# Optimization experiments

Measured on AMD Instinct MI355X. Metric: run time of the kernel, lower is better.

Reference implementation:

```python
import jax, jax.numpy as jnp
import numpy as np

N, S, C, K, V = 8, 2048, 4, 512, 64


def setup_inputs() -> dict:
    key = jax.random.key(0)
    kx, ke = jax.random.split(key)
    x = jax.random.normal(kx, (N, S, C, V), dtype=jnp.float32)
    # nn.Parameter(torch.rand(...)) -> uniform [0,1)
    embedding = jax.random.uniform(ke, (C, K, V), dtype=jnp.float32)
    return {"x": x, "embedding": embedding}


def reference(x, embedding):
    n, s, c, v = x.shape
    xf = x.reshape(n * s, c, v)  # (NS, C, V)
    x2 = jnp.sum(xf * xf, axis=-1, keepdims=True)           # (NS, C, 1)
    e2 = jnp.sum(embedding * embedding, axis=-1)            # (C, K)
    xe = jnp.einsum('ncv,ckv->nck', xf, embedding)          # (NS, C, K)
    d2 = x2 - 2.0 * xe + e2[None]                           # (NS, C, K)
    index = jnp.argmin(d2, axis=2)                          # (NS, C)
    # gather: output[n, c] = embedding[c, index[n, c]]
    output = embedding[jnp.arange(c)[None, :], index]       # (NS, C, V)
    output = output.reshape(x.shape)
    out0 = jax.lax.stop_gradient(output - x) + x            # straight-through
    d1 = jax.lax.stop_gradient(x) - output
    out1 = jnp.sum(d1 * d1, axis=3)                         # (N, S, C)
    d2_ = x - jax.lax.stop_gradient(output)
    out2 = jnp.sum(d2_ * d2_, axis=3)                       # (N, S, C)
    return (out0, out1, out2)
```

## Files before the change

kernel.cpp:

```cpp
#include <hip/hip_runtime.h>

#define NROW 16384
#define CCH  4
#define KCB  512
#define VDIM 64

typedef __attribute__((ext_vector_type(8))) short  short8;
typedef __attribute__((ext_vector_type(4))) float  floatx4;

__device__ inline unsigned short bf16h(float v, float* rem) {
    unsigned u = __float_as_uint(v);
    unsigned r = u + 0x7FFFu + ((u >> 16) & 1u);
    unsigned short h = (unsigned short)(r >> 16);
    *rem = v - __uint_as_float((unsigned)h << 16);
    return h;
}
__device__ inline unsigned short bf16r(float v) {
    unsigned u = __float_as_uint(v);
    return (unsigned short)((u + 0x7FFFu + ((u >> 16) & 1u)) >> 16);
}

__global__ __launch_bounds__(512, 4)
void vq_fused(const float* __restrict__ x, const float* __restrict__ emb,
              float* __restrict__ out) {
    extern __shared__ unsigned short smem[];
    unsigned short* eh = smem;
    float* e2s = (float*)(smem + 32768);

    const int tid  = threadIdx.x;
    const int lane = tid & 63;
    const int m    = lane & 15;
    const int quad = lane >> 4;
    const int wave = tid >> 6;
    const int c    = blockIdx.y;
    const int rbase = blockIdx.x * 128 + wave * 16;

    const float* embc = emb + (size_t)c * (KCB * VDIM);

    {
        const int cb = wave * 64;
        const int koct = m >> 1, half = m & 1;
#pragma unroll
        for (int j = 0; j < 16; ++j) {
            const int g = cb * 16 + j * 64 + lane;
            const float4 t = ((const float4*)embc)[g];
            const int code = cb + j * 4 + quad;
            ushort4 h4;
            h4.x = bf16r(t.x); h4.y = bf16r(t.y);
            h4.z = bf16r(t.z); h4.w = bf16r(t.w);
            const int off = (koct * 512 + (code ^ koct)) * 8 + half * 4;
            *(ushort4*)&eh[off] = h4;
            float s = 0.f;
            s = fmaf(t.x, t.x, s); s = fmaf(t.y, t.y, s);
            s = fmaf(t.z, t.z, s); s = fmaf(t.w, t.w, s);
            s += __shfl_xor(s, 1, 64);
            s += __shfl_xor(s, 2, 64);
            s += __shfl_xor(s, 4, 64);
            s += __shfl_xor(s, 8, 64);
            if (m == 0) e2s[code] = s;
        }
    }

    short8 ah[2], al[2];
    {
        const int row = rbase + m;
        const float4* xr = (const float4*)(x + ((size_t)row * CCH + c) * VDIM);
#pragma unroll
        for (int h = 0; h < 2; ++h) {
            const float4 f0 = xr[h * 8 + quad * 2];
            const float4 f1 = xr[h * 8 + quad * 2 + 1];
            const float fv[8] = {f0.x, f0.y, f0.z, f0.w, f1.x, f1.y, f1.z, f1.w};
            short8 hh, ll;
#pragma unroll
            for (int j = 0; j < 8; ++j) {
                float r, d;
                hh[j] = (short)bf16h(fv[j], &r);
                ll[j] = (short)bf16h(r, &d);
            }
            ah[h] = hh; al[h] = ll;
        }
    }

    __syncthreads();

    float bd[4]; int bkk[4];
#pragma unroll
    for (int j = 0; j < 4; ++j) { bd[j] = 3.4e38f; bkk[j] = 0; }

    const int mq0 = m ^ quad;
    const int mq1 = m ^ (quad + 4);

#pragma unroll 4
    for (int t = 0; t < KCB / 16; ++t) {
        const int code = t * 16 + m;
        const short8 bh0 = *(const short8*)&eh[( quad      * 512 + t * 16 + mq0) * 8];
        const short8 bh1 = *(const short8*)&eh[((quad + 4) * 512 + t * 16 + mq1) * 8];
        const float e2v = e2s[code];

        floatx4 acc0 = {0.f,0.f,0.f,0.f}, acc1 = {0.f,0.f,0.f,0.f};
        acc0 = __builtin_amdgcn_mfma_f32_16x16x32_bf16(ah[0], bh0, acc0, 0, 0, 0);
        acc1 = __builtin_amdgcn_mfma_f32_16x16x32_bf16(al[0], bh0, acc1, 0, 0, 0);
        acc0 = __builtin_amdgcn_mfma_f32_16x16x32_bf16(ah[1], bh1, acc0, 0, 0, 0);
        acc1 = __builtin_amdgcn_mfma_f32_16x16x32_bf16(al[1], bh1, acc1, 0, 0, 0);

#pragma unroll
        for (int j = 0; j < 4; ++j) {
            const float d0 = fmaf(-2.0f, acc0[j] + acc1[j], e2v);
            if (d0 < bd[j]) { bd[j] = d0; bkk[j] = code; }
        }
    }

#pragma unroll
    for (int j = 0; j < 4; ++j) {
        float d = bd[j]; int k = bkk[j];
#pragma unroll
        for (int mask = 1; mask < 16; mask <<= 1) {
            const float od = __shfl_xor(d, mask, 64);
            const int   ok = __shfl_xor(k, mask, 64);
            if (od < d || (od == d && ok < k)) { d = od; k = ok; }
        }
        bd[j] = d; bkk[j] = k;
    }

    const size_t base1 = (size_t)NROW * CCH * VDIM;
    const size_t base2 = base1 + (size_t)NROW * CCH;
#pragma unroll
    for (int j = 0; j < 4; ++j) {
        const int row  = rbase + quad * 4 + j;
        const int code = bkk[j];
        const float4 t4 = ((const float4*)(x + ((size_t)row * CCH + c) * VDIM))[m];
        const float4 e4 = ((const float4*)(embc + (size_t)code * VDIM))[m];
        float4 w;
        w.x = (e4.x - t4.x) + t4.x;
        w.y = (e4.y - t4.y) + t4.y;
        w.z = (e4.z - t4.z) + t4.z;
        w.w = (e4.w - t4.w) + t4.w;
        ((float4*)(out + ((size_t)row * CCH + c) * VDIM))[m] = w;
        float s = 0.f, dx;
        dx = t4.x - e4.x; s = fmaf(dx, dx, s);
        dx = t4.y - e4.y; s = fmaf(dx, dx, s);
        dx = t4.z - e4.z; s = fmaf(dx, dx, s);
        dx = t4.w - e4.w; s = fmaf(dx, dx, s);
        s += __shfl_xor(s, 1, 64);
        s += __shfl_xor(s, 2, 64);
        s += __shfl_xor(s, 4, 64);
        s += __shfl_xor(s, 8, 64);
        if (m == 0) {
            const size_t idx = (size_t)row * CCH + c;
            out[base1 + idx] = s;
            out[base2 + idx] = s;
        }
    }
}

extern "C" void kernel_launch(void* const* d_in, const int* in_sizes, int n_in,
                              void* d_out, int out_size, void* d_ws, size_t ws_size,
                              hipStream_t stream) {
    const float* x   = (const float*)d_in[0];
    const float* emb = (const float*)d_in[1];
    float* out = (float*)d_out;
    const size_t lds_bytes = 65536u + 2048u;
    vq_fused<<<dim3(NROW / 128, CCH), dim3(512), lds_bytes, stream>>>(x, emb, out);
}
```

Before: 85.33 us.

## Split codebook search across two wave groups per row tile and merge via LDS

Each block now handles 64 rows instead of 128, and its eight waves form two groups that each scan half of the codebook (256 codes) for the same 16-row tiles. The two partial argmin results go through shared memory, and the first group merges them and writes the outputs. This halves the serial codebook loop per wave and doubles the grid. The cost is that every block still converts and stages the full codebook into LDS, so that staging work is done twice as often overall, plus an extra barrier. The x row fragments are also loaded twice.

```diff
diff --git a/kernel.cpp b/kernel.cpp
--- a/kernel.cpp
+++ b/kernel.cpp
@@ -23,17 +23,21 @@
 __global__ __launch_bounds__(512, 4)
 void vq_fused(const float* __restrict__ x, const float* __restrict__ emb,
               float* __restrict__ out) {
-    extern __shared__ unsigned short smem[];
-    unsigned short* eh = smem;
-    float* e2s = (float*)(smem + 32768);
+    extern __shared__ char smem[];
+    unsigned short* eh  = (unsigned short*)smem;
+    float*          e2s = (float*)(smem + 65536);
+    float*          sdm = (float*)(smem + 67584);
+    int*            skm = (int*)  (smem + 68096);
 
     const int tid  = threadIdx.x;
     const int lane = tid & 63;
     const int m    = lane & 15;
     const int quad = lane >> 4;
     const int wave = tid >> 6;
+    const int z    = wave >> 2;
+    const int wb   = wave & 3;
     const int c    = blockIdx.y;
-    const int rbase = blockIdx.x * 128 + wave * 16;
+    const int rbase = blockIdx.x * 64 + wb * 16;
 
     const float* embc = emb + (size_t)c * (KCB * VDIM);
 
@@ -87,14 +91,15 @@
 #pragma unroll
     for (int j = 0; j < 4; ++j) { bd[j] = 3.4e38f; bkk[j] = 0; }
 
-    const int mq0 = m ^ quad;
-    const int mq1 = m ^ (quad + 4);
+    const int mq0 = m ^ quad, mq1 = m ^ (quad + 4);
+    const int kbase = z * 256;
 
 #pragma unroll 4
-    for (int t = 0; t < KCB / 16; ++t) {
-        const int code = t * 16 + m;
-        const short8 bh0 = *(const short8*)&eh[( quad      * 512 + t * 16 + mq0) * 8];
-        const short8 bh1 = *(const short8*)&eh[((quad + 4) * 512 + t * 16 + mq1) * 8];
+    for (int t = 0; t < 16; ++t) {
+        const int kb = kbase + t * 16;
+        const int code = kb + m;
+        const short8 bh0 = *(const short8*)&eh[( quad      * 512 + kb + mq0) * 8];
+        const short8 bh1 = *(const short8*)&eh[((quad + 4) * 512 + kb + mq1) * 8];
         const float e2v = e2s[code];
 
         floatx4 acc0 = {0.f,0.f,0.f,0.f}, acc1 = {0.f,0.f,0.f,0.f};
@@ -122,33 +127,50 @@
         bd[j] = d; bkk[j] = k;
     }
 
-    const size_t base1 = (size_t)NROW * CCH * VDIM;
-    const size_t base2 = base1 + (size_t)NROW * CCH;
+    if (m == 0) {
 #pragma unroll
-    for (int j = 0; j < 4; ++j) {
-        const int row  = rbase + quad * 4 + j;
-        const int code = bkk[j];
-        const float4 t4 = ((const float4*)(x + ((size_t)row * CCH + c) * VDIM))[m];
-        const float4 e4 = ((const float4*)(embc + (size_t)code * VDIM))[m];
-        float4 w;
-        w.x = (e4.x - t4.x) + t4.x;
-        w.y = (e4.y - t4.y) + t4.y;
-        w.z = (e4.z - t4.z) + t4.z;
-        w.w = (e4.w - t4.w) + t4.w;
-        ((float4*)(out + ((size_t)row * CCH + c) * VDIM))[m] = w;
-        float s = 0.f, dx;
-        dx = t4.x - e4.x; s = fmaf(dx, dx, s);
-        dx = t4.y - e4.y; s = fmaf(dx, dx, s);
-        dx = t4.z - e4.z; s = fmaf(dx, dx, s);
-        dx = t4.w - e4.w; s = fmaf(dx, dx, s);
-        s += __shfl_xor(s, 1, 64);
-        s += __shfl_xor(s, 2, 64);
-        s += __shfl_xor(s, 4, 64);
-        s += __shfl_xor(s, 8, 64);
-        if (m == 0) {
-            const size_t idx = (size_t)row * CCH + c;
-            out[base1 + idx] = s;
-            out[base2 + idx] = s;
+        for (int j = 0; j < 4; ++j) {
+            sdm[(z * 4 + wb) * 16 + quad * 4 + j] = bd[j];
+            skm[(z * 4 + wb) * 16 + quad * 4 + j] = bkk[j];
+        }
+    }
+    __syncthreads();
+
+    if (z == 0) {
+        const size_t base1 = (size_t)NROW * CCH * VDIM;
+        const size_t base2 = base1 + (size_t)NROW * CCH;
+#pragma unroll
+        for (int j = 0; j < 4; ++j) {
+            const int rl = quad * 4 + j;
+            const float d0 = sdm[ wb      * 16 + rl];
+            const float d1 = sdm[(4 + wb) * 16 + rl];
+            const int   k0 = skm[ wb      * 16 + rl];
+            const int   k1 = skm[(4 + wb) * 16 + rl];
+            const int code = (d1 < d0) ? k1 : k0;
+            const int row  = rbase + rl;
+
+            const float4 t4 = ((const float4*)(x + ((size_t)row * CCH + c) * VDIM))[m];
+            const float4 e4 = ((const float4*)(embc + (size_t)code * VDIM))[m];
+            float4 w;
+            w.x = (e4.x - t4.x) + t4.x;
+            w.y = (e4.y - t4.y) + t4.y;
+            w.z = (e4.z - t4.z) + t4.z;
+            w.w = (e4.w - t4.w) + t4.w;
+            ((float4*)(out + ((size_t)row * CCH + c) * VDIM))[m] = w;
+            float s = 0.f, dx;
+            dx = t4.x - e4.x; s = fmaf(dx, dx, s);
+            dx = t4.y - e4.y; s = fmaf(dx, dx, s);
+            dx = t4.z - e4.z; s = fmaf(dx, dx, s);
+            dx = t4.w - e4.w; s = fmaf(dx, dx, s);
+            s += __shfl_xor(s, 1, 64);
+            s += __shfl_xor(s, 2, 64);
+            s += __shfl_xor(s, 4, 64);
+            s += __shfl_xor(s, 8, 64);
+            if (m == 0) {
+                const size_t idx = (size_t)row * CCH + c;
+                out[base1 + idx] = s;
+                out[base2 + idx] = s;
+            }
         }
     }
 }
@@ -159,6 +181,6 @@
     const float* x   = (const float*)d_in[0];
     const float* emb = (const float*)d_in[1];
     float* out = (float*)d_out;
-    const size_t lds_bytes = 65536u + 2048u;
-    vq_fused<<<dim3(NROW / 128, CCH), dim3(512), lds_bytes, stream>>>(x, emb, out);
+    const size_t lds_bytes = 65536u + 2048u + 512u + 512u;
+    vq_fused<<<dim3(NROW / 64, CCH), dim3(512), lds_bytes, stream>>>(x, emb, out);
 }
```

Measured after the change: 96.15 us. 12.7% more time.
